# Kernel optimization log

Hardware: AMD Instinct MI355X
Metric: run time of the kernel (lower is better)

Reference implementation:

```python
import jax, jax.numpy as jnp
import numpy as np

NL, D, H, DFF = 6, 1024, 16, 4096
HD = D // H


def _rope(x):
    # x: [B, L, H, HD]; rotate-half RoPE applied along seq dim 1
    L = x.shape[1]
    half = HD // 2
    inv = 1.0 / (10000.0 ** (jnp.arange(half, dtype=jnp.float32) / half))
    ang = jnp.arange(L, dtype=jnp.float32)[:, None] * inv  # [L, half]
    cos = jnp.cos(ang)[None, :, None, :]
    sin = jnp.sin(ang)[None, :, None, :]
    x1, x2 = x[..., :half], x[..., half:]
    return jnp.concatenate([x1 * cos - x2 * sin, x1 * sin + x2 * cos], axis=-1)


def _ln(x, eps=1e-5):
    m = jnp.mean(x, axis=-1, keepdims=True)
    v = jnp.var(x, axis=-1, keepdims=True)
    return (x - m) * jax.lax.rsqrt(v + eps)


def _adaln(x, emb, w, b):
    # emb: [B,1,D] -> squeeze; proj -> gamma,beta
    gb = emb[:, 0, :] @ w.T + b  # [B, 2D]
    g, be = jnp.split(gb, 2, axis=-1)
    return _ln(x) * (1.0 + g[:, None, :]) + be[:, None, :]


def _attn(q, k, v, mask):
    # q:[B,Lq,H,HD] k,v:[B,Lkv,H,HD] mask:[B,Lkv] True=ignore
    scores = jnp.einsum('bqhd,bkhd->bhqk', q, k) / np.float32(np.sqrt(HD))
    scores = jnp.where(mask[:, None, None, :], jnp.float32(-jnp.inf), scores)
    w = jax.nn.softmax(scores, axis=-1)
    return jnp.einsum('bhqk,bkhd->bqhd', w, v)


def setup_inputs() -> dict:
    key = jax.random.key(0)
    ks = jax.random.split(key, 20)
    B, L, LC = 4, 1024, 512
    s = 0.02
    inp = {
        'x': jax.random.normal(ks[0], (B, L, D), jnp.float32),
        'noise_emb': jax.random.normal(ks[1], (B, 1, D), jnp.float32),
        'context': jax.random.normal(ks[2], (B, LC, D), jnp.float32),
        'src_mask': jnp.zeros((B, L), bool),
        'ctx_mask': jnp.zeros((B, LC), bool),
        'n1_w': jax.random.normal(ks[3], (NL, 2 * D, D), jnp.float32) * s,
        'n1_b': jnp.zeros((NL, 2 * D), jnp.float32),
        'n2_w': jax.random.normal(ks[4], (NL, 2 * D, D), jnp.float32) * s,
        'n2_b': jnp.zeros((NL, 2 * D), jnp.float32),
        'n3_w': jax.random.normal(ks[5], (NL, 2 * D, D), jnp.float32) * s,
        'n3_b': jnp.zeros((NL, 2 * D), jnp.float32),
        'qkv_w': jax.random.normal(ks[6], (NL, 3 * D, D), jnp.float32) * s,
        'so_w': jax.random.normal(ks[7], (NL, D, D), jnp.float32) * s,
        'cq_w': jax.random.normal(ks[8], (NL, D, D), jnp.float32) * s,
        'ck_w': jax.random.normal(ks[9], (NL, D, D), jnp.float32) * s,
        'cv_w': jax.random.normal(ks[10], (NL, D, D), jnp.float32) * s,
        'co_w': jax.random.normal(ks[11], (NL, D, D), jnp.float32) * s,
        'f1_w': jax.random.normal(ks[12], (NL, DFF, D), jnp.float32) * s,
        'f1_b': jnp.zeros((NL, DFF), jnp.float32),
        'f2_w': jax.random.normal(ks[13], (NL, D, DFF), jnp.float32) * s,
        'f2_b': jnp.zeros((NL, D), jnp.float32),
    }
    return inp


def reference(x, noise_emb, context, src_mask, ctx_mask,
              n1_w, n1_b, n2_w, n2_b, n3_w, n3_b,
              qkv_w, so_w, cq_w, ck_w, cv_w, co_w,
              f1_w, f1_b, f2_w, f2_b):
    B, L, _ = x.shape
    LC = context.shape[1]
    for i in range(NL):
        # self-attention with AdaLN pre-norm
        xn = _adaln(x, noise_emb, n1_w[i], n1_b[i])
        qkv = xn @ qkv_w[i].T  # [B,L,3D]
        q, k, v = jnp.split(qkv, 3, axis=-1)
        q = _rope(q.reshape(B, L, H, HD))
        k = _rope(k.reshape(B, L, H, HD))
        v = v.reshape(B, L, H, HD)
        a = _attn(q, k, v, src_mask).reshape(B, L, D) @ so_w[i].T
        x = x + a
        # cross-attention with AdaLN pre-norm
        xn = _adaln(x, noise_emb, n2_w[i], n2_b[i])
        q = _rope((xn @ cq_w[i].T).reshape(B, L, H, HD))
        k = _rope((context @ ck_w[i].T).reshape(B, LC, H, HD))
        v = (context @ cv_w[i].T).reshape(B, LC, H, HD)
        a = _attn(q, k, v, ctx_mask).reshape(B, L, D) @ co_w[i].T
        x = x + a
        # FFN with AdaLN pre-norm
        xn = _adaln(x, noise_emb, n3_w[i], n3_b[i])
        h = jax.nn.gelu(xn @ f1_w[i].T + f1_b[i], approximate=False)
        x = x + (h @ f2_w[i].T + f2_b[i])
    return x
```

## Files before the change

### kernel.cpp

```cpp
#include <hip/hip_runtime.h>
#include <hip/hip_bf16.h>
#include <math.h>

#define D_    1024
#define H_    16
#define HD_   64
#define NL_   6
#define DFF_  4096
#define B_    4
#define L_    1024
#define LC_   512

typedef short bf16x8 __attribute__((ext_vector_type(8)));
typedef float f32x4  __attribute__((ext_vector_type(4)));
typedef unsigned int uint32;

__device__ __forceinline__ float waveReduceSum(float v) {
#pragma unroll
  for (int off = 32; off > 0; off >>= 1) v += __shfl_xor(v, off);
  return v;
}
__device__ __forceinline__ ushort f2bf(float f) {
  union { __hip_bfloat16 h; ushort u; } c;
  c.h = __float2bfloat16(f);
  return c.u;
}
__device__ __forceinline__ float bf2f(ushort u) {
  union { uint32 i; float f; } c;
  c.i = ((uint32)u) << 16;
  return c.f;
}
__device__ __forceinline__ void gload16(const ushort* g, ushort* l) {
  __builtin_amdgcn_global_load_lds(
      (const __attribute__((address_space(1))) uint32*)g,
      (__attribute__((address_space(3))) uint32*)l, 16, 0, 0);
}

__global__ __launch_bounds__(256) void cvt_bf16_kernel(
    const float* __restrict__ in, ushort* __restrict__ out, int n4) {
  int i = blockIdx.x * 256 + threadIdx.x;
  int stride = gridDim.x * 256;
  for (; i < n4; i += stride) {
    float4 v = ((const float4*)in)[i];
    ushort4 o = {f2bf(v.x), f2bf(v.y), f2bf(v.z), f2bf(v.w)};
    ((ushort4*)out)[i] = o;
  }
}

__global__ __launch_bounds__(256) void cvt_pack_kv_kernel(
    const float* __restrict__ ck, const float* __restrict__ cv,
    ushort* __restrict__ out, int n4) {
  int i = blockIdx.x * 256 + threadIdx.x;
  int stride = gridDim.x * 256;
  for (; i < n4; i += stride) {
    int row = i >> 8;
    int cb = i & 255;
    int layer = row >> 11;
    int sel = (row >> 10) & 1;
    int r = row & 1023;
    const float* src = (sel ? cv : ck) +
                       (((size_t)layer << 10) + r) * 1024 + cb * 4;
    float4 v = *(const float4*)src;
    ushort4 o = {f2bf(v.x), f2bf(v.y), f2bf(v.z), f2bf(v.w)};
    ((ushort4*)out)[i] = o;
  }
}

__global__ void rope_table_kernel(float* __restrict__ tab) {
  int t = blockIdx.x * 256 + threadIdx.x;
  if (t >= L_ * 32) return;
  int l = t >> 5, j = t & 31;
  float inv = powf(10000.f, -(float)j * (1.f / 32.f));
  float ang = (float)l * inv;
  tab[l * 64 + j] = cosf(ang);
  tab[l * 64 + 32 + j] = sinf(ang);
}

__global__ __launch_bounds__(256) void adaln_gb_all_kernel(
    const float* __restrict__ emb,
    const float* __restrict__ n1w, const float* __restrict__ n2w,
    const float* __restrict__ n3w,
    const float* __restrict__ n1b, const float* __restrict__ n2b,
    const float* __restrict__ n3b,
    float* __restrict__ gb) {
  int wid = blockIdx.x * 4 + (threadIdx.x >> 6);
  int lane = threadIdx.x & 63;
  int n = wid & 2047;
  int g = wid >> 11;
  int layer = g / 3, j = g - layer * 3;
  const float* wbase = (j == 0 ? n1w : (j == 1 ? n2w : n3w));
  const float* bbase = (j == 0 ? n1b : (j == 1 ? n2b : n3b));
  const float* wr = wbase + ((size_t)layer * 2048 + n) * 1024;
  float s0 = 0.f, s1 = 0.f, s2 = 0.f, s3 = 0.f;
#pragma unroll
  for (int k4 = 0; k4 < 4; ++k4) {
    int idx = k4 * 64 + lane;
    float4 w4 = ((const float4*)wr)[idx];
    float4 e0 = ((const float4*)emb)[idx];
    float4 e1 = ((const float4*)(emb + 1024))[idx];
    float4 e2 = ((const float4*)(emb + 2048))[idx];
    float4 e3 = ((const float4*)(emb + 3072))[idx];
    s0 += w4.x * e0.x + w4.y * e0.y + w4.z * e0.z + w4.w * e0.w;
    s1 += w4.x * e1.x + w4.y * e1.y + w4.z * e1.z + w4.w * e1.w;
    s2 += w4.x * e2.x + w4.y * e2.y + w4.z * e2.z + w4.w * e2.w;
    s3 += w4.x * e3.x + w4.y * e3.y + w4.z * e3.z + w4.w * e3.w;
  }
  s0 = waveReduceSum(s0);
  s1 = waveReduceSum(s1);
  s2 = waveReduceSum(s2);
  s3 = waveReduceSum(s3);
  if (lane == 0) {
    float bb = bbase[(size_t)layer * 2048 + n];
    gb[((size_t)g * 4 + 0) * 2048 + n] = s0 + bb;
    gb[((size_t)g * 4 + 1) * 2048 + n] = s1 + bb;
    gb[((size_t)g * 4 + 2) * 2048 + n] = s2 + bb;
    gb[((size_t)g * 4 + 3) * 2048 + n] = s3 + bb;
  }
}

__global__ __launch_bounds__(256) void adaln_apply_kernel(
    const float* __restrict__ x, const float* __restrict__ gb,
    ushort* __restrict__ xn) {
  int r = blockIdx.x;
  int b = r >> 10;
  const float* xr = x + (size_t)r * D_;
  int tid = threadIdx.x;
  float4 v = *(const float4*)(xr + tid * 4);
  float s = v.x + v.y + v.z + v.w;
  float q = v.x * v.x + v.y * v.y + v.z * v.z + v.w * v.w;
  s = waveReduceSum(s);
  q = waveReduceSum(q);
  __shared__ float ssum[4], ssq[4], stats[2];
  int w = tid >> 6, lane = tid & 63;
  if (lane == 0) { ssum[w] = s; ssq[w] = q; }
  __syncthreads();
  if (tid == 0) {
    float S = ssum[0] + ssum[1] + ssum[2] + ssum[3];
    float Q = ssq[0] + ssq[1] + ssq[2] + ssq[3];
    float mean = S * (1.f / D_);
    float var = Q * (1.f / D_) - mean * mean;
    stats[0] = mean;
    stats[1] = rsqrtf(var + 1e-5f);
  }
  __syncthreads();
  float mean = stats[0], rstd = stats[1];
  const float* gp = gb + (size_t)b * 2048;
  float4 g  = *(const float4*)(gp + tid * 4);
  float4 be = *(const float4*)(gp + D_ + tid * 4);
  ushort4 o;
  o.x = f2bf((v.x - mean) * rstd * (1.f + g.x) + be.x);
  o.y = f2bf((v.y - mean) * rstd * (1.f + g.y) + be.y);
  o.z = f2bf((v.z - mean) * rstd * (1.f + g.z) + be.z);
  o.w = f2bf((v.w - mean) * rstd * (1.f + g.w) + be.w);
  *(ushort4*)(xn + (size_t)r * D_ + tid * 4) = o;
}

template <int FLAGS, bool OUTBF, int ROPE>
__global__ __launch_bounds__(256) void gemm_mfma_kernel(
    const ushort* __restrict__ A, int lda,
    const ushort* __restrict__ W, int ldw,
    const float* __restrict__ bias,
    const float* __restrict__ res, int ldres,
    void* __restrict__ Cout, int ldc, int K,
    const float* __restrict__ tab, int rlim, int lmask) {
  __shared__ __align__(16) ushort lds[24576];
  const int tid = threadIdx.x;
  const int lane = tid & 63, wv = tid >> 6;
  const int wrow = (wv >> 1) * 64, wcol = (wv & 1) * 64;
  const int fr = lane & 15, kb = (lane >> 4) * 8;

  const int nwg = gridDim.x * gridDim.y;
  const int wg = blockIdx.y * gridDim.x + blockIdx.x;
  const int q = nwg >> 3;
  const int swz = (wg & 7) * q + (wg >> 3);
  const int row0 = (swz / gridDim.x) * 128;
  const int col0 = (swz % gridDim.x) * 128;

  const int c0 = wv * 2, c1 = wv * 2 + 1;
  const int sr = lane >> 2, sc = (lane & 3) * 8;
  const ushort* Ap0 = A + (size_t)(row0 + c0 * 16 + sr) * lda + sc;
  const ushort* Ap1 = A + (size_t)(row0 + c1 * 16 + sr) * lda + sc;
  const ushort* Wp0 = W + (size_t)(col0 + c0 * 16 + sr) * ldw + sc;
  const ushort* Wp1 = W + (size_t)(col0 + c1 * 16 + sr) * ldw + sc;

  f32x4 acc[4][4];
#pragma unroll
  for (int m = 0; m < 4; ++m)
#pragma unroll
    for (int n = 0; n < 4; ++n) acc[m][n] = (f32x4)0.f;

#define ASB(B) (lds + (B) * 4096)
#define WSB(B) (lds + 12288 + (B) * 4096)
#define STAGE(B, T)                                   \
  do {                                                \
    const int koff_ = (T) * 32;                       \
    gload16(Ap0 + koff_, ASB(B) + c0 * 512);          \
    gload16(Ap1 + koff_, ASB(B) + c1 * 512);          \
    gload16(Wp0 + koff_, WSB(B) + c0 * 512);          \
    gload16(Wp1 + koff_, WSB(B) + c1 * 512);          \
  } while (0)
#define WAITV8() asm volatile("s_waitcnt vmcnt(8)" ::: "memory")
#define WAITV4() asm volatile("s_waitcnt vmcnt(4)" ::: "memory")
#define WAITV0() asm volatile("s_waitcnt vmcnt(0)" ::: "memory")
#define BAR()    __builtin_amdgcn_s_barrier()
#define COMPUTE(B)                                                          \
  do {                                                                      \
    bf16x8 af[4], bfr[4];                                                   \
    _Pragma("unroll")                                                       \
    for (int m = 0; m < 4; ++m)                                             \
      af[m] = *(const bf16x8*)(ASB(B) + (wrow + m * 16 + fr) * 32 + kb);    \
    _Pragma("unroll")                                                       \
    for (int n = 0; n < 4; ++n)                                             \
      bfr[n] = *(const bf16x8*)(WSB(B) + (wcol + n * 16 + fr) * 32 + kb);   \
    _Pragma("unroll")                                                       \
    for (int m = 0; m < 4; ++m)                                             \
      _Pragma("unroll")                                                     \
      for (int n = 0; n < 4; ++n)                                           \
        acc[m][n] = __builtin_amdgcn_mfma_f32_16x16x32_bf16(af[m], bfr[n],  \
                                                            acc[m][n], 0, 0, 0); \
  } while (0)

  const int NT = K >> 5;
  STAGE(0, 0);
  STAGE(1, 1);
  for (int t = 0; t < NT; t += 3) {
    {
      const bool sA = (t + 2) < NT;
      if (sA) STAGE(2, t + 2);
      if ((t + 1) < NT) { if (sA) WAITV8(); else WAITV4(); } else WAITV0();
      BAR(); COMPUTE(0); BAR();
    }
    if ((t + 1) < NT) {
      const bool sB = (t + 3) < NT;
      if (sB) STAGE(0, t + 3);
      if ((t + 2) < NT) { if (sB) WAITV8(); else WAITV4(); } else WAITV0();
      BAR(); COMPUTE(1); BAR();
    }
    if ((t + 2) < NT) {
      const bool sC = (t + 4) < NT;
      if (sC) STAGE(1, t + 4);
      if ((t + 3) < NT) { if (sC) WAITV8(); else WAITV4(); } else WAITV0();
      BAR(); COMPUTE(2); BAR();
    }
  }
#undef STAGE
#undef WAITV8
#undef WAITV4
#undef WAITV0
#undef COMPUTE

  float bn[4];
  if (FLAGS & 1) {
#pragma unroll
    for (int n = 0; n < 4; ++n) bn[n] = bias[col0 + wcol + n * 16 + fr];
  }
#define EPI(v, n)                                                     \
  do {                                                                \
    if (FLAGS & 1) (v) += bn[n];                                      \
    if (FLAGS & 2) (v) = 0.5f * (v) * (1.f + erff((v) * 0.70710678118f)); \
  } while (0)

  if (OUTBF) {
    ushort* Ct = lds;
    ushort* Cg = (ushort*)Cout;
#pragma unroll
    for (int m = 0; m < 4; ++m) {
      int lr0 = wrow + m * 16 + (lane >> 4) * 4;
#pragma unroll
      for (int n = 0; n < 4; ++n) {
        int lc = wcol + n * 16 + fr;
#pragma unroll
        for (int r = 0; r < 4; ++r) {
          float v = acc[m][n][r];
          EPI(v, n);
          Ct[(lr0 + r) * 128 + lc] = f2bf(v);
        }
      }
    }
    __syncthreads();
#pragma unroll
    for (int it = 0; it < 8; ++it) {
      int lr = (tid >> 4) + it * 16;
      int lc = (tid & 15) * 8;
      union { int4 v; ushort us[8]; } vv;
      vv.v = *(const int4*)&Ct[lr * 128 + lc];
      if (ROPE && (col0 + lc) < rlim) {
        union { int4 v; ushort us[8]; } pv;
        pv.v = *(const int4*)&Ct[lr * 128 + (lc ^ 32)];
        int l = (row0 + lr) & lmask;
        int j = lc & 31;
        const float* cb = &tab[l * 64 + j];
        bool lowhalf = (lc & 63) < 32;
#pragma unroll
        for (int e = 0; e < 8; ++e) {
          float cc = cb[e], ss = cb[32 + e];
          float xv = bf2f(vv.us[e]), xp = bf2f(pv.us[e]);
          float o = lowhalf ? (xv * cc - xp * ss) : (xp * ss + xv * cc);
          vv.us[e] = f2bf(o);
        }
      }
      *(int4*)&Cg[(size_t)(row0 + lr) * ldc + col0 + lc] = vv.v;
    }
  } else {
    float* Cf = (float*)lds;
    float* Cg = (float*)Cout;
#pragma unroll
    for (int half = 0; half < 2; ++half) {
      if ((wv >> 1) == half) {
#pragma unroll
        for (int m = 0; m < 4; ++m) {
          int lr0 = m * 16 + (lane >> 4) * 4;
#pragma unroll
          for (int n = 0; n < 4; ++n) {
            int lc = wcol + n * 16 + fr;
#pragma unroll
            for (int r = 0; r < 4; ++r) {
              float v = acc[m][n][r];
              EPI(v, n);
              Cf[(lr0 + r) * 128 + lc] = v;
            }
          }
        }
      }
      __syncthreads();
#pragma unroll
      for (int it = 0; it < 8; ++it) {
        int lr = (tid >> 5) + it * 8;
        int lc = (tid & 31) * 4;
        int grow = row0 + half * 64 + lr;
        float4 v = *(const float4*)&Cf[lr * 128 + lc];
        if (FLAGS & 4) {
          float4 rv = *(const float4*)&res[(size_t)grow * ldres + col0 + lc];
          v.x += rv.x; v.y += rv.y; v.z += rv.z; v.w += rv.w;
        }
        *(float4*)&Cg[(size_t)grow * ldc + col0 + lc] = v;
      }
      __syncthreads();
    }
  }
#undef EPI
#undef ASB
#undef WSB
#undef BAR
}

#define SWZ(row, col) (((row) << 6) + ((col) ^ (((row) & 7) << 3)))
__global__ __launch_bounds__(256) void attn_mfma_kernel(
    const ushort* __restrict__ Q, int ldq,
    const ushort* __restrict__ K, int ldk,
    const ushort* __restrict__ V, int ldv,
    ushort* __restrict__ O, int ldo,
    int Lq, int Lk, float scale) {
  __shared__ __align__(16) ushort Ks[2][64 * 64];
  __shared__ __align__(16) ushort Vt[2][64 * 64];
  __shared__ __align__(16) ushort Ps[4][16 * 64];
  const int tid = threadIdx.x;
  const int lane = tid & 63, w = tid >> 6;
  const int fr = lane & 15, hi = lane >> 4, kb = hi * 8;
  const int b = blockIdx.z, h = blockIdx.y, q0 = blockIdx.x * 64;

  bf16x8 aq[2];
  {
    const ushort* qp = Q + (size_t)(b * Lq + q0 + w * 16 + fr) * ldq + h * 64 + kb;
    union { bf16x8 v; ushort us[8]; } t0, t1;
    t0.v = *(const bf16x8*)qp;
    t1.v = *(const bf16x8*)(qp + 32);
#pragma unroll
    for (int e = 0; e < 8; ++e) {
      t0.us[e] = f2bf(bf2f(t0.us[e]) * scale);
      t1.us[e] = f2bf(bf2f(t1.us[e]) * scale);
    }
    aq[0] = t0.v;
    aq[1] = t1.v;
  }

  const ushort* kbase = K + (size_t)(b * Lk + lane) * ldk + h * 64 + w * 16;
  const ushort* vbase = V + (size_t)(b * Lk + lane) * ldv + h * 64 + w * 16;
  int4 kr0, kr1, vr0, vr1;
#define LOADKV(T)                                          \
  do {                                                     \
    const ushort* kp_ = kbase + (size_t)(T) * 64 * ldk;    \
    kr0 = ((const int4*)kp_)[0];                           \
    kr1 = ((const int4*)kp_)[1];                           \
    const ushort* vp_ = vbase + (size_t)(T) * 64 * ldv;    \
    vr0 = ((const int4*)vp_)[0];                           \
    vr1 = ((const int4*)vp_)[1];                           \
  } while (0)
#define WRITEKV(P)                                                   \
  do {                                                               \
    *(int4*)&Ks[P][SWZ(lane, w * 16)]     = kr0;                     \
    *(int4*)&Ks[P][SWZ(lane, w * 16 + 8)] = kr1;                     \
    union { int4 v; ushort us[8]; } u0_, u1_;                        \
    u0_.v = vr0; u1_.v = vr1;                                        \
    _Pragma("unroll")                                                \
    for (int e = 0; e < 8; ++e) Vt[P][SWZ(w * 16 + e, lane)] = u0_.us[e]; \
    _Pragma("unroll")                                                \
    for (int e = 0; e < 8; ++e) Vt[P][SWZ(w * 16 + 8 + e, lane)] = u1_.us[e]; \
  } while (0)

  f32x4 oacc[4];
#pragma unroll
  for (int n = 0; n < 4; ++n) oacc[n] = (f32x4)0.f;
  float mq = -1e30f, lq = 0.f;
  const int ntiles = Lk >> 6;

  LOADKV(0);
  WRITEKV(0);
  int p = 0;
  for (int t = 0; t < ntiles; ++t) {
    if (t + 1 < ntiles) LOADKV(t + 1);
    __syncthreads();

    f32x4 sacc[4];
#pragma unroll
    for (int n = 0; n < 4; ++n) sacc[n] = (f32x4)0.f;
#pragma unroll
    for (int s = 0; s < 2; ++s) {
#pragma unroll
      for (int n = 0; n < 4; ++n) {
        bf16x8 ak = *(const bf16x8*)&Ks[p][SWZ(n * 16 + fr, s * 32 + kb)];
        sacc[n] = __builtin_amdgcn_mfma_f32_16x16x32_bf16(ak, aq[s], sacc[n], 0, 0, 0);
      }
    }

    float sm = sacc[0][0];
#pragma unroll
    for (int n = 0; n < 4; ++n)
#pragma unroll
      for (int r = 0; r < 4; ++r) sm = fmaxf(sm, sacc[n][r]);
    sm = fmaxf(sm, __shfl_xor(sm, 16));
    sm = fmaxf(sm, __shfl_xor(sm, 32));
    float mnew = fmaxf(mq, sm);
    float corrq = __expf(mq - mnew);
    mq = mnew;
    float psum = 0.f;
#pragma unroll
    for (int n = 0; n < 4; ++n) {
#pragma unroll
      for (int r = 0; r < 4; ++r) {
        float pe = __expf(sacc[n][r] - mnew);
        psum += pe;
        Ps[w][SWZ(fr, n * 16 + hi * 4 + r)] = f2bf(pe);
      }
    }
    psum += __shfl_xor(psum, 16);
    psum += __shfl_xor(psum, 32);
    lq = lq * corrq + psum;
    float c0 = __shfl(corrq, hi * 4 + 0);
    float c1 = __shfl(corrq, hi * 4 + 1);
    float c2 = __shfl(corrq, hi * 4 + 2);
    float c3 = __shfl(corrq, hi * 4 + 3);
#pragma unroll
    for (int n = 0; n < 4; ++n) {
      oacc[n][0] *= c0; oacc[n][1] *= c1; oacc[n][2] *= c2; oacc[n][3] *= c3;
    }

#pragma unroll
    for (int s = 0; s < 2; ++s) {
      bf16x8 pa = *(const bf16x8*)&Ps[w][SWZ(fr, s * 32 + kb)];
#pragma unroll
      for (int n = 0; n < 4; ++n) {
        bf16x8 bv = *(const bf16x8*)&Vt[p][SWZ(n * 16 + fr, s * 32 + kb)];
        oacc[n] = __builtin_amdgcn_mfma_f32_16x16x32_bf16(pa, bv, oacc[n], 0, 0, 0);
      }
    }

    __syncthreads();
    if (t + 1 < ntiles) WRITEKV(p ^ 1);
    p ^= 1;
  }
#undef LOADKV
#undef WRITEKV

  float linv[4];
#pragma unroll
  for (int r = 0; r < 4; ++r) linv[r] = 1.f / __shfl(lq, hi * 4 + r);
  ushort* Os = &Ps[0][0];
#pragma unroll
  for (int r = 0; r < 4; ++r) {
    int rl = w * 16 + hi * 4 + r;
#pragma unroll
    for (int n = 0; n < 4; ++n)
      Os[SWZ(rl, n * 16 + fr)] = f2bf(oacc[n][r] * linv[r]);
  }
  __syncthreads();
  {
    int row = tid >> 2, cbk = (tid & 3) * 16;
    ushort* op = O + (size_t)(b * Lq + q0 + row) * ldo + h * 64 + cbk;
    int4 o0 = *(const int4*)&Os[SWZ(row, cbk)];
    int4 o1 = *(const int4*)&Os[SWZ(row, cbk + 8)];
    ((int4*)op)[0] = o0;
    ((int4*)op)[1] = o1;
  }
}

extern "C" void kernel_launch(void* const* d_in, const int* in_sizes, int n_in,
                              void* d_out, int out_size, void* d_ws, size_t ws_size,
                              hipStream_t stream) {
  const float* x_in = (const float*)d_in[0];
  const float* emb  = (const float*)d_in[1];
  const float* ctx  = (const float*)d_in[2];
  const float* n1w = (const float*)d_in[5];
  const float* n1b = (const float*)d_in[6];
  const float* n2w = (const float*)d_in[7];
  const float* n2b = (const float*)d_in[8];
  const float* n3w = (const float*)d_in[9];
  const float* n3b = (const float*)d_in[10];
  const float* qkvw = (const float*)d_in[11];
  const float* sow  = (const float*)d_in[12];
  const float* cqw  = (const float*)d_in[13];
  const float* ckw  = (const float*)d_in[14];
  const float* cvw  = (const float*)d_in[15];
  const float* cow  = (const float*)d_in[16];
  const float* f1w  = (const float*)d_in[17];
  const float* f1b  = (const float*)d_in[18];
  const float* f2w  = (const float*)d_in[19];
  const float* f2b  = (const float*)d_in[20];

  float* xcur = (float*)d_out;

  ushort* xnb  = (ushort*)d_ws;
  ushort* big  = xnb + (size_t)4096 * 1024;
  ushort* obb  = big + (size_t)4096 * 4096;
  ushort* kvb  = obb + (size_t)4096 * 1024;
  ushort* ctxb = kvb + (size_t)2048 * 2048;
  float*  gball= (float*)(ctxb + (size_t)2048 * 1024);
  float*  tab  = gball + 18 * 4 * 2048;
  ushort* scrW = (ushort*)(tab + 65536);
  const size_t SZ_QKV = (size_t)NL_ * 3072 * 1024;
  const size_t SZ_SQ  = (size_t)NL_ * 1024 * 1024;
  const size_t SZ_F   = (size_t)NL_ * 4096 * 1024;
  ushort* wqkv = scrW + (size_t)4096 * 1024;
  ushort* wso  = wqkv + SZ_QKV;
  ushort* wcq  = wso + SZ_SQ;
  ushort* wkv  = wcq + SZ_SQ;
  ushort* wco  = wkv + 2 * SZ_SQ;
  ushort* wf1  = wco + SZ_SQ;
  ushort* wf2  = wf1 + SZ_F;
  const size_t need_full = (size_t)((char*)(wf2 + SZ_F) - (char*)d_ws);
  const bool wbfull = (ws_size >= need_full);

  hipMemcpyAsync(xcur, x_in, (size_t)B_ * L_ * D_ * sizeof(float),
                 hipMemcpyDeviceToDevice, stream);
  rope_table_kernel<<<128, 256, 0, stream>>>(tab);
  adaln_gb_all_kernel<<<9216, 256, 0, stream>>>(emb, n1w, n2w, n3w,
                                                n1b, n2b, n3b, gball);
  cvt_bf16_kernel<<<1024, 256, 0, stream>>>(ctx, ctxb,
                                            (int)((size_t)2048 * 1024 / 4));

  if (wbfull) {
    cvt_bf16_kernel<<<2048, 256, 0, stream>>>(qkvw, wqkv, (int)(SZ_QKV / 4));
    cvt_bf16_kernel<<<2048, 256, 0, stream>>>(sow,  wso,  (int)(SZ_SQ / 4));
    cvt_bf16_kernel<<<2048, 256, 0, stream>>>(cqw,  wcq,  (int)(SZ_SQ / 4));
    cvt_pack_kv_kernel<<<2048, 256, 0, stream>>>(ckw, cvw, wkv,
                                                 (int)(2 * SZ_SQ / 4));
    cvt_bf16_kernel<<<2048, 256, 0, stream>>>(cow,  wco,  (int)(SZ_SQ / 4));
    cvt_bf16_kernel<<<2048, 256, 0, stream>>>(f1w,  wf1,  (int)(SZ_F / 4));
    cvt_bf16_kernel<<<2048, 256, 0, stream>>>(f2w,  wf2,  (int)(SZ_F / 4));
  }

  auto prepW = [&](const float* src, ushort* full, size_t layerOff,
                   size_t nelem) -> const ushort* {
    if (wbfull) return full + layerOff;
    cvt_bf16_kernel<<<1024, 256, 0, stream>>>(src + layerOff, scrW,
                                              (int)(nelem / 4));
    return scrW;
  };

  const int ROWS = B_ * L_;
  const dim3 blk(256);

  for (int i = 0; i < NL_; ++i) {
    const float* f1bi = f1b + (size_t)i * DFF_;
    const float* f2bi = f2b + (size_t)i * D_;

    adaln_apply_kernel<<<ROWS, blk, 0, stream>>>(
        xcur, gball + (size_t)(i * 3 + 0) * 4 * 2048, xnb);
    gemm_mfma_kernel<0, true, 1><<<dim3(24, 32), blk, 0, stream>>>(
        xnb, D_, prepW(qkvw, wqkv, (size_t)i * 3072 * 1024, (size_t)3072 * 1024),
        D_, nullptr, nullptr, 0, big, 3072, D_, tab, 2048, 1023);
    attn_mfma_kernel<<<dim3(L_ / 64, H_, B_), blk, 0, stream>>>(
        big, 3072, big + 1024, 3072, big + 2048, 3072, obb, D_, L_, L_, 0.125f);
    gemm_mfma_kernel<4, false, 0><<<dim3(8, 32), blk, 0, stream>>>(
        obb, D_, prepW(sow, wso, (size_t)i * 1024 * 1024, (size_t)1024 * 1024),
        D_, nullptr, xcur, D_, xcur, D_, D_, tab, 0, 0);

    adaln_apply_kernel<<<ROWS, blk, 0, stream>>>(
        xcur, gball + (size_t)(i * 3 + 1) * 4 * 2048, xnb);
    gemm_mfma_kernel<0, true, 1><<<dim3(8, 32), blk, 0, stream>>>(
        xnb, D_, prepW(cqw, wcq, (size_t)i * 1024 * 1024, (size_t)1024 * 1024),
        D_, nullptr, nullptr, 0, big, 1024, D_, tab, 1024, 1023);
    {
      const ushort* wkvi;
      if (wbfull) {
        wkvi = wkv + (size_t)i * 2048 * 1024;
      } else {
        cvt_bf16_kernel<<<512, 256, 0, stream>>>(
            ckw + (size_t)i * 1024 * 1024, scrW, (int)((size_t)1024 * 1024 / 4));
        cvt_bf16_kernel<<<512, 256, 0, stream>>>(
            cvw + (size_t)i * 1024 * 1024, scrW + (size_t)1024 * 1024,
            (int)((size_t)1024 * 1024 / 4));
        wkvi = scrW;
      }
      gemm_mfma_kernel<0, true, 1><<<dim3(16, 16), blk, 0, stream>>>(
          ctxb, D_, wkvi, D_, nullptr, nullptr, 0, kvb, 2048, D_, tab, 1024, 511);
    }
    attn_mfma_kernel<<<dim3(L_ / 64, H_, B_), blk, 0, stream>>>(
        big, 1024, kvb, 2048, kvb + 1024, 2048, obb, D_, L_, LC_, 0.125f);
    gemm_mfma_kernel<4, false, 0><<<dim3(8, 32), blk, 0, stream>>>(
        obb, D_, prepW(cow, wco, (size_t)i * 1024 * 1024, (size_t)1024 * 1024),
        D_, nullptr, xcur, D_, xcur, D_, D_, tab, 0, 0);

    adaln_apply_kernel<<<ROWS, blk, 0, stream>>>(
        xcur, gball + (size_t)(i * 3 + 2) * 4 * 2048, xnb);
    gemm_mfma_kernel<3, true, 0><<<dim3(32, 32), blk, 0, stream>>>(
        xnb, D_, prepW(f1w, wf1, (size_t)i * 4096 * 1024, (size_t)4096 * 1024),
        D_, f1bi, nullptr, 0, big, DFF_, D_, tab, 0, 0);
    gemm_mfma_kernel<5, false, 0><<<dim3(8, 32), blk, 0, stream>>>(
        big, DFF_, prepW(f2w, wf2, (size_t)i * 4096 * 1024, (size_t)4096 * 1024),
        DFF_, f2bi, xcur, D_, xcur, D_, DFF_, tab, 0, 0);
  }
}
```

Before: 2.194 ms.

## Swizzle GEMM LDS tiles, pad epilogue staging, and shuffle attention probabilities in registers

The GEMM's LDS A/W tiles now use an XOR swizzle on the k-chunk, applied both to the global-to-LDS load address and to the fragment reads. The epilogue staging buffers get padded row strides to reduce LDS bank conflicts. In attention, the softmax probabilities no longer round-trip through LDS. Each lane packs them to bf16 and rebuilds the MFMA A-operand with cross-lane shuffles, and s_setprio is raised around the MFMA blocks. This trades LDS traffic and conflicts for extra shuffles and selects, and the new register-permutation mapping has to match the old LDS layout exactly.

```diff
diff --git a/kernel.cpp b/kernel.cpp
--- a/kernel.cpp
+++ b/kernel.cpp
@@ -29,6 +29,9 @@
   union { uint32 i; float f; } c;
   c.i = ((uint32)u) << 16;
   return c.f;
+}
+__device__ __forceinline__ uint32 pk2(float a, float b) {
+  return (uint32)f2bf(a) | ((uint32)f2bf(b) << 16);
 }
 __device__ __forceinline__ void gload16(const ushort* g, ushort* l) {
   __builtin_amdgcn_global_load_lds(
@@ -167,7 +170,8 @@
   const int tid = threadIdx.x;
   const int lane = tid & 63, wv = tid >> 6;
   const int wrow = (wv >> 1) * 64, wcol = (wv & 1) * 64;
-  const int fr = lane & 15, kb = (lane >> 4) * 8;
+  const int fr = lane & 15;
+  const int kbs = (((lane >> 4) ^ (fr & 3)) & 3) * 8;
 
   const int nwg = gridDim.x * gridDim.y;
   const int wg = blockIdx.y * gridDim.x + blockIdx.x;
@@ -177,7 +181,8 @@
   const int col0 = (swz % gridDim.x) * 128;
 
   const int c0 = wv * 2, c1 = wv * 2 + 1;
-  const int sr = lane >> 2, sc = (lane & 3) * 8;
+  const int sr = lane >> 2;
+  const int sc = (((lane & 3) ^ (sr & 3)) & 3) * 8;
   const ushort* Ap0 = A + (size_t)(row0 + c0 * 16 + sr) * lda + sc;
   const ushort* Ap1 = A + (size_t)(row0 + c1 * 16 + sr) * lda + sc;
   const ushort* Wp0 = W + (size_t)(col0 + c0 * 16 + sr) * ldw + sc;
@@ -208,10 +213,10 @@
     bf16x8 af[4], bfr[4];                                                   \
     _Pragma("unroll")                                                       \
     for (int m = 0; m < 4; ++m)                                             \
-      af[m] = *(const bf16x8*)(ASB(B) + (wrow + m * 16 + fr) * 32 + kb);    \
+      af[m] = *(const bf16x8*)(ASB(B) + (wrow + m * 16 + fr) * 32 + kbs);   \
     _Pragma("unroll")                                                       \
     for (int n = 0; n < 4; ++n)                                             \
-      bfr[n] = *(const bf16x8*)(WSB(B) + (wcol + n * 16 + fr) * 32 + kb);   \
+      bfr[n] = *(const bf16x8*)(WSB(B) + (wcol + n * 16 + fr) * 32 + kbs);  \
     _Pragma("unroll")                                                       \
     for (int m = 0; m < 4; ++m)                                             \
       _Pragma("unroll")                                                     \
@@ -273,7 +278,7 @@
         for (int r = 0; r < 4; ++r) {
           float v = acc[m][n][r];
           EPI(v, n);
-          Ct[(lr0 + r) * 128 + lc] = f2bf(v);
+          Ct[(lr0 + r) * 136 + lc] = f2bf(v);
         }
       }
     }
@@ -283,10 +288,10 @@
       int lr = (tid >> 4) + it * 16;
       int lc = (tid & 15) * 8;
       union { int4 v; ushort us[8]; } vv;
-      vv.v = *(const int4*)&Ct[lr * 128 + lc];
+      vv.v = *(const int4*)&Ct[lr * 136 + lc];
       if (ROPE && (col0 + lc) < rlim) {
         union { int4 v; ushort us[8]; } pv;
-        pv.v = *(const int4*)&Ct[lr * 128 + (lc ^ 32)];
+        pv.v = *(const int4*)&Ct[lr * 136 + (lc ^ 32)];
         int l = (row0 + lr) & lmask;
         int j = lc & 31;
         const float* cb = &tab[l * 64 + j];
@@ -317,7 +322,7 @@
             for (int r = 0; r < 4; ++r) {
               float v = acc[m][n][r];
               EPI(v, n);
-              Cf[(lr0 + r) * 128 + lc] = v;
+              Cf[(lr0 + r) * 132 + lc] = v;
             }
           }
         }
@@ -328,7 +333,7 @@
         int lr = (tid >> 5) + it * 8;
         int lc = (tid & 31) * 4;
         int grow = row0 + half * 64 + lr;
-        float4 v = *(const float4*)&Cf[lr * 128 + lc];
+        float4 v = *(const float4*)&Cf[lr * 132 + lc];
         if (FLAGS & 4) {
           float4 rv = *(const float4*)&res[(size_t)grow * ldres + col0 + lc];
           v.x += rv.x; v.y += rv.y; v.z += rv.z; v.w += rv.w;
@@ -353,7 +358,7 @@
     int Lq, int Lk, float scale) {
   __shared__ __align__(16) ushort Ks[2][64 * 64];
   __shared__ __align__(16) ushort Vt[2][64 * 64];
-  __shared__ __align__(16) ushort Ps[4][16 * 64];
+  __shared__ __align__(16) ushort Os[64 * 64];
   const int tid = threadIdx.x;
   const int lane = tid & 63, w = tid >> 6;
   const int fr = lane & 15, hi = lane >> 4, kb = hi * 8;
@@ -403,6 +408,8 @@
   for (int n = 0; n < 4; ++n) oacc[n] = (f32x4)0.f;
   float mq = -1e30f, lq = 0.f;
   const int ntiles = Lk >> 6;
+  const bool lowhalf = (lane < 32);
+  const bool sendSelf = (hi == 1 || hi == 2);
 
   LOADKV(0);
   WRITEKV(0);
@@ -414,6 +421,7 @@
     f32x4 sacc[4];
 #pragma unroll
     for (int n = 0; n < 4; ++n) sacc[n] = (f32x4)0.f;
+    __builtin_amdgcn_s_setprio(1);
 #pragma unroll
     for (int s = 0; s < 2; ++s) {
 #pragma unroll
@@ -422,6 +430,7 @@
         sacc[n] = __builtin_amdgcn_mfma_f32_16x16x32_bf16(ak, aq[s], sacc[n], 0, 0, 0);
       }
     }
+    __builtin_amdgcn_s_setprio(0);
 
     float sm = sacc[0][0];
 #pragma unroll
@@ -433,16 +442,15 @@
     float mnew = fmaxf(mq, sm);
     float corrq = __expf(mq - mnew);
     mq = mnew;
+    float pe[4][4];
     float psum = 0.f;
 #pragma unroll
-    for (int n = 0; n < 4; ++n) {
+    for (int n = 0; n < 4; ++n)
 #pragma unroll
       for (int r = 0; r < 4; ++r) {
-        float pe = __expf(sacc[n][r] - mnew);
-        psum += pe;
-        Ps[w][SWZ(fr, n * 16 + hi * 4 + r)] = f2bf(pe);
+        pe[n][r] = __expf(sacc[n][r] - mnew);
+        psum += pe[n][r];
       }
-    }
     psum += __shfl_xor(psum, 16);
     psum += __shfl_xor(psum, 32);
     lq = lq * corrq + psum;
@@ -455,15 +463,54 @@
       oacc[n][0] *= c0; oacc[n][1] *= c1; oacc[n][2] *= c2; oacc[n][3] *= c3;
     }
 
-#pragma unroll
-    for (int s = 0; s < 2; ++s) {
-      bf16x8 pa = *(const bf16x8*)&Ps[w][SWZ(fr, s * 32 + kb)];
-#pragma unroll
-      for (int n = 0; n < 4; ++n) {
-        bf16x8 bv = *(const bf16x8*)&Vt[p][SWZ(n * 16 + fr, s * 32 + kb)];
-        oacc[n] = __builtin_amdgcn_mfma_f32_16x16x32_bf16(pa, bv, oacc[n], 0, 0, 0);
-      }
-    }
+    uint32 u00 = pk2(pe[0][0], pe[0][1]), u01 = pk2(pe[0][2], pe[0][3]);
+    uint32 u10 = pk2(pe[1][0], pe[1][1]), u11 = pk2(pe[1][2], pe[1][3]);
+    uint32 u20 = pk2(pe[2][0], pe[2][1]), u21 = pk2(pe[2][2], pe[2][3]);
+    uint32 u30 = pk2(pe[3][0], pe[3][1]), u31 = pk2(pe[3][2], pe[3][3]);
+    uint32 selfw0 = lowhalf ? u00 : u10;
+    uint32 selfw1 = lowhalf ? u01 : u11;
+    uint32 selfw2 = lowhalf ? u20 : u30;
+    uint32 selfw3 = lowhalf ? u21 : u31;
+    uint32 send10 = lowhalf ? u10 : u00;
+    uint32 send11 = lowhalf ? u11 : u01;
+    uint32 send12 = lowhalf ? u30 : u20;
+    uint32 send13 = lowhalf ? u31 : u21;
+    uint32 farw0 = __shfl_xor((int)send10, 32);
+    uint32 farw1 = __shfl_xor((int)send11, 32);
+    uint32 farw2 = __shfl_xor((int)send12, 32);
+    uint32 farw3 = __shfl_xor((int)send13, 32);
+    uint32 s20 = sendSelf ? selfw0 : farw0;
+    uint32 s21 = sendSelf ? selfw1 : farw1;
+    uint32 s22 = sendSelf ? selfw2 : farw2;
+    uint32 s23 = sendSelf ? selfw3 : farw3;
+    uint32 rcv0 = __shfl_xor((int)s20, 16);
+    uint32 rcv1 = __shfl_xor((int)s21, 16);
+    uint32 rcv2 = __shfl_xor((int)s22, 16);
+    uint32 rcv3 = __shfl_xor((int)s23, 16);
+    union { uint32 wd[4]; bf16x8 v; } pa0, pa1;
+    if (hi == 0) {
+      pa0.wd[0] = selfw0; pa0.wd[1] = selfw1; pa0.wd[2] = rcv0; pa0.wd[3] = rcv1;
+      pa1.wd[0] = selfw2; pa1.wd[1] = selfw3; pa1.wd[2] = rcv2; pa1.wd[3] = rcv3;
+    } else if (hi == 1) {
+      pa0.wd[0] = rcv0; pa0.wd[1] = rcv1; pa0.wd[2] = farw0; pa0.wd[3] = farw1;
+      pa1.wd[0] = rcv2; pa1.wd[1] = rcv3; pa1.wd[2] = farw2; pa1.wd[3] = farw3;
+    } else if (hi == 2) {
+      pa0.wd[0] = farw0; pa0.wd[1] = farw1; pa0.wd[2] = rcv0; pa0.wd[3] = rcv1;
+      pa1.wd[0] = farw2; pa1.wd[1] = farw3; pa1.wd[2] = rcv2; pa1.wd[3] = rcv3;
+    } else {
+      pa0.wd[0] = rcv0; pa0.wd[1] = rcv1; pa0.wd[2] = selfw0; pa0.wd[3] = selfw1;
+      pa1.wd[0] = rcv2; pa1.wd[1] = rcv3; pa1.wd[2] = selfw2; pa1.wd[3] = selfw3;
+    }
+
+    __builtin_amdgcn_s_setprio(1);
+#pragma unroll
+    for (int n = 0; n < 4; ++n) {
+      bf16x8 bv0 = *(const bf16x8*)&Vt[p][SWZ(n * 16 + fr, 0 * 32 + kb)];
+      oacc[n] = __builtin_amdgcn_mfma_f32_16x16x32_bf16(pa0.v, bv0, oacc[n], 0, 0, 0);
+      bf16x8 bv1 = *(const bf16x8*)&Vt[p][SWZ(n * 16 + fr, 1 * 32 + kb)];
+      oacc[n] = __builtin_amdgcn_mfma_f32_16x16x32_bf16(pa1.v, bv1, oacc[n], 0, 0, 0);
+    }
+    __builtin_amdgcn_s_setprio(0);
 
     __syncthreads();
     if (t + 1 < ntiles) WRITEKV(p ^ 1);
@@ -475,7 +522,6 @@
   float linv[4];
 #pragma unroll
   for (int r = 0; r < 4; ++r) linv[r] = 1.f / __shfl(lq, hi * 4 + r);
-  ushort* Os = &Ps[0][0];
 #pragma unroll
   for (int r = 0; r < 4; ++r) {
     int rl = w * 16 + hi * 4 + r;
```

New measurement: 2.167 ms. Within noise of the previous version (-1.2%).
